# Kernel tuning notes

Hardware: AMD Instinct MI355X
Metric: run time of the kernel (lower is better)

The kernel has to match this reference:

```python
import jax, jax.numpy as jnp
import numpy as np

N_HEAD = 16
D_HEAD = 64
D_MODEL = 1024
N_ROLL = 3
SCALE = 1.0 / (D_HEAD ** 0.5)
EPS = 1e-5


def mul_roll_repeat(x, n_roll):
    # concat of x * roll(x, i) over i=1..n_roll along last dim
    return jnp.concatenate([x * jnp.roll(x, i, axis=-1) for i in range(1, n_roll + 1)], axis=-1)


def dpfp(x):
    # DPFP feature map: [relu(x), relu(-x)] then roll-multiply-repeat
    x2 = jnp.concatenate([jax.nn.relu(x), jax.nn.relu(-x)], axis=-1)
    return mul_roll_repeat(x2, N_ROLL)


def layer_norm(x, gamma, beta):
    mu = jnp.mean(x, axis=-1, keepdims=True)
    var = jnp.var(x, axis=-1, keepdims=True)
    return (x - mu) * jax.lax.rsqrt(var + 1e-5) * gamma + beta


def setup_inputs() -> dict:
    key = jax.random.key(0)
    ks = jax.random.split(key, 4)
    S, B = 2048, 2
    h = jax.random.normal(ks[0], (S, B, D_MODEL), dtype=jnp.float32)
    Wq = jax.random.normal(ks[1], (D_MODEL, N_HEAD * D_HEAD), dtype=jnp.float32) * 0.02
    Wkv = jax.random.normal(ks[2], (D_MODEL, 2 * N_HEAD * D_HEAD), dtype=jnp.float32) * 0.02
    Wo = jax.random.normal(ks[3], (N_HEAD * D_HEAD, D_MODEL), dtype=jnp.float32) * 0.02
    ln_gamma = jnp.ones((D_MODEL,), dtype=jnp.float32)
    ln_beta = jnp.zeros((D_MODEL,), dtype=jnp.float32)
    return {"h": h, "Wq": Wq, "Wkv": Wkv, "Wo": Wo, "ln_gamma": ln_gamma, "ln_beta": ln_beta}


def reference(h, Wq, Wkv, Wo, ln_gamma, ln_beta):
    # h: [S, B, D_MODEL]; mems=None, attn_mask=None, post-LN, eval (no dropout)
    S, B, _ = h.shape
    q = (h @ Wq).reshape(S, B, N_HEAD, D_HEAD)
    kv = h @ Wkv
    k, v = jnp.split(kv, 2, axis=-1)
    k = k.reshape(S, B, N_HEAD, D_HEAD)
    v = v.reshape(S, B, N_HEAD, D_HEAD)

    pq = dpfp(q)  # [S, B, N, F], F = 2*D_HEAD*N_ROLL = 384
    pk = dpfp(k)

    # Linear-attention form: identical math to the original quadratic
    # einsum('ibnd,jbnd->ijbn') * scale, summed over j for the denominator,
    # since there is no mask and dropatt=0. Avoids the O(S^2) score tensor.
    kv_agg = jnp.einsum('jbnf,jbnd->bnfd', pk, v)          # [B, N, F, D]
    z = pk.sum(axis=0)                                      # [B, N, F]
    num = jnp.einsum('ibnf,bnfd->ibnd', pq, kv_agg) * SCALE  # [S, B, N, D]
    den = jnp.einsum('ibnf,bnf->ibn', pq, z) * SCALE + EPS   # [S, B, N]
    attn_vec = (num / den[..., None]).reshape(S, B, N_HEAD * D_HEAD)

    attn_out = attn_vec @ Wo
    return layer_norm(h + attn_out, ln_gamma, ln_beta)
```

## Files before the change

### kernel.cpp

```cpp
#include <hip/hip_runtime.h>
#include <math.h>

#define NH 16
#define DM 1024
#define FEAT 384
#define SB 4096
#define SEQ 2048

static constexpr float SCALE = 0.125f;
static constexpr float EPS = 1e-5f;

typedef __attribute__((ext_vector_type(8))) _Float16 half8;
typedef __attribute__((ext_vector_type(4))) _Float16 half4;
typedef __attribute__((ext_vector_type(4))) float f32x4;

#define AS1 __attribute__((address_space(1)))
#define AS3 __attribute__((address_space(3)))

#define IDX(r, o) ((((r) << 6)) + ((((o) ^ ((r) & 7))) << 3))

__global__ __launch_bounds__(256) void prep_kernel(const float* __restrict__ h,
                                                   const float* __restrict__ Wq,
                                                   const float* __restrict__ Wkv,
                                                   const float* __restrict__ Wo,
                                                   _Float16* __restrict__ h_h,
                                                   _Float16* __restrict__ WqkvT,
                                                   _Float16* __restrict__ WoT) {
    __shared__ _Float16 tile[32][33];
    int bid = blockIdx.x, t = threadIdx.x;
    if (bid < 4096) {
        int i = bid * 256 + t;
        const float4 v = ((const float4*)h)[i];
        half4 o = {(_Float16)v.x, (_Float16)v.y, (_Float16)v.z, (_Float16)v.w};
        ((half4*)h_h)[i] = o;
        return;
    }
    const float* src;
    _Float16* dst;
    int N, col0, n0, k0;
    if (bid < 7168) {
        int b2 = bid - 4096;
        n0 = (b2 % 96) * 32; k0 = (b2 / 96) * 32;
        if (n0 < 1024) { src = Wq; N = 1024; col0 = n0; }
        else           { src = Wkv; N = 2048; col0 = n0 - 1024; }
        dst = WqkvT;
    } else {
        int b3 = bid - 7168;
        n0 = (b3 & 31) * 32; k0 = (b3 >> 5) * 32;
        src = Wo; N = 1024; col0 = n0; dst = WoT;
    }
    int tx = t & 31, ty = t >> 5;
    #pragma unroll
    for (int i = 0; i < 4; ++i)
        tile[ty + i * 8][tx] = (_Float16)src[(size_t)(k0 + ty + i * 8) * N + col0 + tx];
    __syncthreads();
    #pragma unroll
    for (int i = 0; i < 4; ++i)
        dst[(size_t)(n0 + ty + i * 8) * 1024 + k0 + tx] = tile[tx][ty + i * 8];
}

__global__ __launch_bounds__(512) void gemm_qkv(const _Float16* __restrict__ A,
                                                const _Float16* __restrict__ BT,
                                                _Float16* __restrict__ C,
                                                int M, int N, int K) {
    __shared__ _Float16 smem[57344];
    const int t = threadIdx.x;
    const int w = t >> 6, l = t & 63;
    const int wr = w >> 1, wc = w & 1;
    const int NT = K >> 6;

    int nwg = gridDim.x;
    int cpx = nwg >> 3;
    int bid = blockIdx.x;
    int swz = (bid & 7) * cpx + (bid >> 3);
    int ntile = N / 192;
    int row0 = (swz / ntile) << 8;
    int col0 = (swz % ntile) * 192;

    f32x4 acc[4][6];
    #pragma unroll
    for (int m = 0; m < 4; ++m)
        #pragma unroll
        for (int n = 0; n < 6; ++n)
            acc[m][n] = (f32x4){0.f, 0.f, 0.f, 0.f};

    const int lr = l >> 3;
    const int lc8 = ((l & 7) ^ lr) * 8;

    auto STAGE_TILE = [&](int tau) {
        if (tau >= NT) return;
        int kk = tau << 6;
        int bufo = (tau & 1) * 28672;
        #pragma unroll
        for (int i = 0; i < 2; ++i) {
            int chunk = w * 2 + i;
            const _Float16* src = BT + (size_t)(col0 + chunk * 8 + lr) * K + kk + lc8;
            __builtin_amdgcn_global_load_lds((const AS1 void*)src,
                (AS3 void*)(smem + bufo + 16384 + chunk * 512), 16, 0, 0);
        }
        {
            const _Float16* src = BT + (size_t)(col0 + 128 + w * 8 + lr) * K + kk + lc8;
            __builtin_amdgcn_global_load_lds((const AS1 void*)src,
                (AS3 void*)(smem + bufo + 24576 + w * 512), 16, 0, 0);
        }
        #pragma unroll
        for (int i = 0; i < 4; ++i) {
            int chunk = w * 4 + i;
            const _Float16* src = A + (size_t)(row0 + chunk * 8 + lr) * K + kk + lc8;
            __builtin_amdgcn_global_load_lds((const AS1 void*)src,
                (AS3 void*)(smem + bufo + chunk * 512), 16, 0, 0);
        }
    };

    STAGE_TILE(0);
    asm volatile("s_waitcnt vmcnt(0)" ::: "memory");
    __builtin_amdgcn_s_barrier();

    #pragma unroll 1
    for (int ti = 0; ti < NT; ++ti) {
        const int bufo = (ti & 1) * 28672;
        STAGE_TILE(ti + 1);
        half8 a[4][2], bv[6][2];
        #pragma unroll
        for (int mf = 0; mf < 4; ++mf) {
            int r = wr * 64 + mf * 16 + (l & 15);
            #pragma unroll
            for (int ks = 0; ks < 2; ++ks) {
                int c16 = (ks * 4 + (l >> 4)) ^ (r & 7);
                a[mf][ks] = *(const half8*)&smem[bufo + r * 64 + c16 * 8];
            }
        }
        #pragma unroll
        for (int nf = 0; nf < 6; ++nf) {
            int r = wc * 96 + nf * 16 + (l & 15);
            #pragma unroll
            for (int ks = 0; ks < 2; ++ks) {
                int c16 = (ks * 4 + (l >> 4)) ^ (r & 7);
                bv[nf][ks] = *(const half8*)&smem[bufo + 16384 + r * 64 + c16 * 8];
            }
        }
        __builtin_amdgcn_sched_barrier(0);
        asm volatile("s_waitcnt lgkmcnt(0)" ::: "memory");
        __builtin_amdgcn_sched_barrier(0);
        __builtin_amdgcn_s_setprio(1);
        #pragma unroll
        for (int mf = 0; mf < 4; ++mf)
            #pragma unroll
            for (int nf = 0; nf < 6; ++nf)
                #pragma unroll
                for (int ks = 0; ks < 2; ++ks)
                    acc[mf][nf] = __builtin_amdgcn_mfma_f32_16x16x32_f16(
                        a[mf][ks], bv[nf][ks], acc[mf][nf], 0, 0, 0);
        __builtin_amdgcn_s_setprio(0);
        __builtin_amdgcn_sched_barrier(0);
        asm volatile("s_waitcnt vmcnt(0)" ::: "memory");
        __builtin_amdgcn_s_barrier();
    }

    int ocol = l & 15, orow4 = (l >> 4) * 4;
    #pragma unroll
    for (int mf = 0; mf < 4; ++mf)
        #pragma unroll
        for (int nf = 0; nf < 6; ++nf) {
            size_t base = (size_t)(row0 + wr * 64 + mf * 16 + orow4) * N
                        + col0 + wc * 96 + nf * 16 + ocol;
            #pragma unroll
            for (int j = 0; j < 4; ++j)
                C[base + (size_t)j * N] = (_Float16)acc[mf][nf][j];
        }
}

__global__ __launch_bounds__(256) void gemm_wo(const _Float16* __restrict__ A,
                                               const _Float16* __restrict__ BT,
                                               _Float16* __restrict__ C,
                                               int M, int N, int K) {
    __shared__ _Float16 smem[3 * 16384];
    const int t = threadIdx.x;
    const int w = t >> 6, l = t & 63;
    const int wr = w >> 1, wc = w & 1;
    const int NT = K >> 6;
    int row0 = blockIdx.y * 128, col0 = blockIdx.x * 128;

    f32x4 acc[4][4];
    #pragma unroll
    for (int m = 0; m < 4; ++m)
        #pragma unroll
        for (int n = 0; n < 4; ++n)
            acc[m][n] = (f32x4){0.f, 0.f, 0.f, 0.f};

    const int lr = l >> 3;
    const int lc8 = ((l & 7) ^ lr) * 8;

    auto STAGE = [&](int ti) {
        if (ti >= NT) return;
        int kk = ti << 6;
        int bufo = (ti % 3) * 16384;
        #pragma unroll
        for (int i = 0; i < 4; ++i) {
            int chunk = w * 4 + i;
            const _Float16* asrc = A + (size_t)(row0 + chunk * 8 + lr) * K + kk + lc8;
            __builtin_amdgcn_global_load_lds((const AS1 void*)asrc,
                (AS3 void*)(smem + bufo + chunk * 512), 16, 0, 0);
            const _Float16* bsrc = BT + (size_t)(col0 + chunk * 8 + lr) * K + kk + lc8;
            __builtin_amdgcn_global_load_lds((const AS1 void*)bsrc,
                (AS3 void*)(smem + bufo + 8192 + chunk * 512), 16, 0, 0);
        }
    };

    STAGE(0); STAGE(1);
    asm volatile("s_waitcnt vmcnt(8)" ::: "memory");
    __builtin_amdgcn_s_barrier();

    #pragma unroll 1
    for (int ti = 0; ti < NT; ++ti) {
        const int bufo = (ti % 3) * 16384;
        half8 a[4][2], bv[4][2];
        #pragma unroll
        for (int mf = 0; mf < 4; ++mf) {
            int r = wr * 64 + mf * 16 + (l & 15);
            #pragma unroll
            for (int ks = 0; ks < 2; ++ks) {
                int c16 = (ks * 4 + (l >> 4)) ^ (r & 7);
                a[mf][ks] = *(const half8*)&smem[bufo + r * 64 + c16 * 8];
            }
        }
        #pragma unroll
        for (int nf = 0; nf < 4; ++nf) {
            int r = wc * 64 + nf * 16 + (l & 15);
            #pragma unroll
            for (int ks = 0; ks < 2; ++ks) {
                int c16 = (ks * 4 + (l >> 4)) ^ (r & 7);
                bv[nf][ks] = *(const half8*)&smem[bufo + 8192 + r * 64 + c16 * 8];
            }
        }
        STAGE(ti + 2);
        __builtin_amdgcn_sched_barrier(0);
        asm volatile("s_waitcnt lgkmcnt(0)" ::: "memory");
        __builtin_amdgcn_sched_barrier(0);
        __builtin_amdgcn_s_setprio(1);
        #pragma unroll
        for (int mf = 0; mf < 4; ++mf)
            #pragma unroll
            for (int nf = 0; nf < 4; ++nf)
                #pragma unroll
                for (int ks = 0; ks < 2; ++ks)
                    acc[mf][nf] = __builtin_amdgcn_mfma_f32_16x16x32_f16(
                        a[mf][ks], bv[nf][ks], acc[mf][nf], 0, 0, 0);
        __builtin_amdgcn_s_setprio(0);
        __builtin_amdgcn_sched_barrier(0);
        if (ti < NT - 2) asm volatile("s_waitcnt vmcnt(8)" ::: "memory");
        else             asm volatile("s_waitcnt vmcnt(0)" ::: "memory");
        __builtin_amdgcn_s_barrier();
    }

    int ocol = l & 15, orow = (l >> 4) * 4;
    #pragma unroll
    for (int mf = 0; mf < 4; ++mf)
        #pragma unroll
        for (int nf = 0; nf < 4; ++nf) {
            size_t base = (size_t)(row0 + wr * 64 + mf * 16 + orow) * N
                        + col0 + wc * 64 + nf * 16 + ocol;
            #pragma unroll
            for (int j = 0; j < 4; ++j)
                C[base + (size_t)j * N] = (_Float16)acc[mf][nf][j];
        }
}

__global__ __launch_bounds__(512) void kvagg_fused(const _Float16* __restrict__ qkv,
                                                   _Float16* __restrict__ kvp,
                                                   float* __restrict__ zp) {
    __shared__ _Float16 x2s[128 * 64];
    __shared__ _Float16 vTs[64 * 64];
    __shared__ _Float16 pkTs[384 * 64];
    const int t = threadIdx.x;
    const int w = t >> 6, l = t & 63;
    const int bn = blockIdx.x;
    const int jseg = blockIdx.y;
    const int b = bn >> 4, nh = bn & 15;

    f32x4 acc[4][3];
    #pragma unroll
    for (int mf = 0; mf < 4; ++mf)
        #pragma unroll
        for (int nf = 0; nf < 3; ++nf)
            acc[mf][nf] = (f32x4){0.f, 0.f, 0.f, 0.f};
    float zacc[3] = {0.f, 0.f, 0.f};

    const int sc = t & 63;
    const int so = t >> 6;

    #pragma unroll 1
    for (int ch = 0; ch < 4; ++ch) {
        int j0 = jseg * 256 + ch * 64;
        _Float16 kx[8], vx[8];
        #pragma unroll
        for (int e = 0; e < 8; ++e) {
            size_t rb = (size_t)((j0 + so * 8 + e) * 2 + b) * 3072 + nh * 64 + sc;
            kx[e] = qkv[rb + 1024];
            vx[e] = qkv[rb + 2048];
        }
        half8 xlo, xhi, vv;
        #pragma unroll
        for (int e = 0; e < 8; ++e) {
            float kf = (float)kx[e];
            xlo[e] = (_Float16)fmaxf(kf, 0.f);
            xhi[e] = (_Float16)fmaxf(-kf, 0.f);
            vv[e] = vx[e];
        }
        if (ch) __syncthreads();
        *(half8*)&x2s[IDX(sc, so)] = xlo;
        *(half8*)&x2s[IDX(sc + 64, so)] = xhi;
        *(half8*)&vTs[IDX(sc, so)] = vv;
        __syncthreads();
        {
            const int o = t & 7;
            const int fb = t >> 3;
            #pragma unroll
            for (int it = 0; it < 6; ++it) {
                int f = it * 64 + fb;
                int fm = f & 127;
                int r = (f >> 7) + 1;
                int fm2 = (fm - r) & 127;
                half8 pa = *(const half8*)&x2s[IDX(fm, o)];
                half8 pb = *(const half8*)&x2s[IDX(fm2, o)];
                *(half8*)&pkTs[IDX(f, o)] = pa * pb;
            }
        }
        __syncthreads();
        #pragma unroll
        for (int ks = 0; ks < 2; ++ks) {
            half8 a[4], bq[3];
            int oo = ks * 4 + (l >> 4);
            #pragma unroll
            for (int mf = 0; mf < 4; ++mf) {
                int dr = mf * 16 + (l & 15);
                a[mf] = *(const half8*)&vTs[IDX(dr, oo)];
            }
            #pragma unroll
            for (int nf = 0; nf < 3; ++nf) {
                int fr = w * 48 + nf * 16 + (l & 15);
                bq[nf] = *(const half8*)&pkTs[IDX(fr, oo)];
                #pragma unroll
                for (int e = 0; e < 8; ++e) zacc[nf] += (float)bq[nf][e];
            }
            #pragma unroll
            for (int mf = 0; mf < 4; ++mf)
                #pragma unroll
                for (int nf = 0; nf < 3; ++nf)
                    acc[mf][nf] = __builtin_amdgcn_mfma_f32_16x16x32_f16(
                        a[mf], bq[nf], acc[mf][nf], 0, 0, 0);
        }
    }

    #pragma unroll
    for (int nf = 0; nf < 3; ++nf) {
        float v = zacc[nf];
        v += __shfl_xor(v, 16, 64);
        v += __shfl_xor(v, 32, 64);
        if (l < 16)
            zp[(size_t)(jseg * 32 + bn) * FEAT + w * 48 + nf * 16 + l] = v;
    }
    _Float16* outp = kvp + (size_t)(jseg * 32 + bn) * 64 * FEAT;
    int orow = (l >> 4) * 4, ocol = l & 15;
    #pragma unroll
    for (int mf = 0; mf < 4; ++mf)
        #pragma unroll
        for (int nf = 0; nf < 3; ++nf) {
            int fcol = w * 48 + nf * 16 + ocol;
            #pragma unroll
            for (int j = 0; j < 4; ++j)
                outp[(size_t)(mf * 16 + orow + j) * FEAT + fcol] = (_Float16)acc[mf][nf][j];
        }
}

__global__ __launch_bounds__(256) void reduceA(const _Float16* __restrict__ kvp,
                                               const float* __restrict__ zp,
                                               _Float16* __restrict__ kvaggT,
                                               float* __restrict__ z) {
    const int NKV = 32 * 64 * FEAT;
    int idx = blockIdx.x * 256 + threadIdx.x;
    if (idx < NKV) {
        float s = 0.f;
        #pragma unroll
        for (int c = 0; c < 8; ++c) s += (float)kvp[(size_t)c * NKV + idx];
        kvaggT[idx] = (_Float16)s;
    } else if (idx < NKV + 32 * FEAT) {
        int e = idx - NKV;
        float s = 0.f;
        #pragma unroll
        for (int c = 0; c < 8; ++c) s += zp[c * 32 * FEAT + e];
        z[e] = s;
    }
}

#define X2STR 152
__global__ __launch_bounds__(256) void attn_fused(const _Float16* __restrict__ qkv,
                                                  const _Float16* __restrict__ kvaggT,
                                                  const float* __restrict__ z,
                                                  _Float16* __restrict__ av) {
    __shared__ _Float16 x2e[64 * X2STR];
    __shared__ _Float16 B_lds[64 * FEAT];
    __shared__ float z_lds[FEAT];
    __shared__ float den_lds[64];
    const int t = threadIdx.x;
    const int w = t >> 6, l = t & 63;
    const int iblk = blockIdx.x;
    const int bn = blockIdx.y;
    const int b = bn >> 4, nh = bn & 15;

    {
        const _Float16* Bg = kvaggT + (size_t)bn * 64 * FEAT;
        #pragma unroll
        for (int s = 0; s < 12; ++s) {
            int idx8 = t + 256 * s;
            int row = idx8 / 48, c16 = idx8 - row * 48;
            half8 vv = *(const half8*)&Bg[row * FEAT + c16 * 8];
            *(half8*)&B_lds[row * FEAT + ((c16 ^ (row & 7)) << 3)] = vv;
        }
    }
    for (int e = t; e < FEAT; e += 256) z_lds[e] = z[(size_t)bn * FEAT + e];

    {
        int row = t >> 2, c0 = (t & 3) * 16;
        const _Float16* qrow = qkv + (size_t)((iblk * 64 + row) * 2 + b) * 3072 + nh * 64;
        half8 q0 = *(const half8*)&qrow[c0];
        half8 q1 = *(const half8*)&qrow[c0 + 8];
        half8 lo0, lo1, hi0, hi1;
        #pragma unroll
        for (int e = 0; e < 8; ++e) {
            float f0 = (float)q0[e], f1 = (float)q1[e];
            lo0[e] = (_Float16)fmaxf(f0, 0.f);
            lo1[e] = (_Float16)fmaxf(f1, 0.f);
            hi0[e] = (_Float16)fmaxf(-f0, 0.f);
            hi1[e] = (_Float16)fmaxf(-f1, 0.f);
        }
        _Float16* xr = &x2e[row * X2STR];
        *(half8*)&xr[c0] = lo0;
        *(half8*)&xr[c0 + 8] = lo1;
        *(half8*)&xr[64 + c0] = hi0;
        *(half8*)&xr[64 + c0 + 8] = hi1;
        if (c0 == 0) { *(half8*)&xr[128] = lo0; *(half8*)&xr[136] = lo1; }
        if (c0 == 16) { *(half8*)&xr[144] = lo0; }
    }
    __syncthreads();

    const int rloc16 = l & 15;
    const int csel = (l >> 4) * 8;
    const int lrow = w * 16 + rloc16;
    half8 y8[16];
    {
        const _Float16* xr = &x2e[lrow * X2STR + csel];
        #pragma unroll
        for (int j = 0; j < 16; ++j)
            y8[j] = *(const half8*)&xr[j * 8];
    }
    half8 afr[12];
    #pragma unroll
    for (int ks = 0; ks < 12; ++ks) {
        const int r = (ks >> 2) + 1;
        #pragma unroll
        for (int e = 0; e < 8; ++e) {
            const int j1 = ((ks & 3) * 32 + e) & 127;
            const int j2 = ((ks & 3) * 32 + e - r) & 127;
            afr[ks][e] = y8[j1 >> 3][j1 & 7] * y8[j2 >> 3][j2 & 7];
        }
    }

    f32x4 acc[4];
    #pragma unroll
    for (int n = 0; n < 4; ++n) acc[n] = (f32x4){0.f, 0.f, 0.f, 0.f};
    float den = 0.f;
    #pragma unroll
    for (int ks = 0; ks < 12; ++ks) {
        const float4 z0 = *(const float4*)&z_lds[ks * 32 + csel];
        const float4 z1 = *(const float4*)&z_lds[ks * 32 + csel + 4];
        den += (float)afr[ks][0] * z0.x + (float)afr[ks][1] * z0.y
             + (float)afr[ks][2] * z0.z + (float)afr[ks][3] * z0.w
             + (float)afr[ks][4] * z1.x + (float)afr[ks][5] * z1.y
             + (float)afr[ks][6] * z1.z + (float)afr[ks][7] * z1.w;
        #pragma unroll
        for (int nf = 0; nf < 4; ++nf) {
            int row = nf * 16 + rloc16;
            int c16 = (ks * 4 + (l >> 4)) ^ (row & 7);
            half8 bfr = *(const half8*)&B_lds[row * FEAT + (c16 << 3)];
            acc[nf] = __builtin_amdgcn_mfma_f32_16x16x32_f16(afr[ks], bfr, acc[nf], 0, 0, 0);
        }
    }

    den += __shfl_xor(den, 16, 64);
    den += __shfl_xor(den, 32, 64);
    if (l < 16) den_lds[w * 16 + l] = den;
    __syncthreads();

    #pragma unroll
    for (int nf = 0; nf < 4; ++nf)
        #pragma unroll
        for (int j = 0; j < 4; ++j) {
            int rl = w * 16 + (l >> 4) * 4 + j;
            float dv = den_lds[rl] * SCALE + EPS;
            float val = acc[nf][j] * SCALE / dv;
            int i = iblk * 64 + rl;
            av[((size_t)i * 2 + b) * 1024 + nh * 64 + nf * 16 + (l & 15)] = (_Float16)val;
        }
}

__global__ __launch_bounds__(256) void ln_kernel(const float* __restrict__ h,
                                                 const _Float16* __restrict__ attn_out,
                                                 const float* __restrict__ gamma,
                                                 const float* __restrict__ beta,
                                                 float* __restrict__ out) {
    int r = blockIdx.x;
    int t = threadIdx.x;
    const float4 hv = ((const float4*)(h + (size_t)r * 1024))[t];
    const half4 a4 = ((const half4*)(attn_out + (size_t)r * 1024))[t];
    float x[4] = {hv.x + (float)a4[0], hv.y + (float)a4[1],
                  hv.z + (float)a4[2], hv.w + (float)a4[3]};
    float sum = x[0] + x[1] + x[2] + x[3];
    float sq = x[0]*x[0] + x[1]*x[1] + x[2]*x[2] + x[3]*x[3];
    #pragma unroll
    for (int off = 32; off >= 1; off >>= 1) {
        sum += __shfl_xor(sum, off, 64);
        sq += __shfl_xor(sq, off, 64);
    }
    __shared__ float ssum[4], ssq[4];
    int wl = t >> 6, lane = t & 63;
    if (lane == 0) { ssum[wl] = sum; ssq[wl] = sq; }
    __syncthreads();
    sum = ssum[0] + ssum[1] + ssum[2] + ssum[3];
    sq = ssq[0] + ssq[1] + ssq[2] + ssq[3];
    float mu = sum * (1.f / 1024.f);
    float var = sq * (1.f / 1024.f) - mu * mu;
    float rs = rsqrtf(var + 1e-5f);
    const float4 g4 = ((const float4*)gamma)[t];
    const float4 b4 = ((const float4*)beta)[t];
    float4 o;
    o.x = (x[0] - mu) * rs * g4.x + b4.x;
    o.y = (x[1] - mu) * rs * g4.y + b4.y;
    o.z = (x[2] - mu) * rs * g4.z + b4.z;
    o.w = (x[3] - mu) * rs * g4.w + b4.w;
    ((float4*)(out + (size_t)r * 1024))[t] = o;
}

extern "C" void kernel_launch(void* const* d_in, const int* in_sizes, int n_in,
                              void* d_out, int out_size, void* d_ws, size_t ws_size,
                              hipStream_t stream) {
    const float* h     = (const float*)d_in[0];
    const float* Wq    = (const float*)d_in[1];
    const float* Wkv   = (const float*)d_in[2];
    const float* Wo    = (const float*)d_in[3];
    const float* gamma = (const float*)d_in[4];
    const float* beta  = (const float*)d_in[5];
    float* out = (float*)d_out;
    _Float16* u = (_Float16*)d_ws;

    _Float16* h_h    = u;
    _Float16* WqkvT  = u + 4194304;
    _Float16* WoT    = u + 7340032;
    _Float16* qkv    = u + 8388608;
    _Float16* kvp    = u + 20971520;
    float*    zp     = (float*)(u + 33554432);
    _Float16* kvaggT = u + 33751040;
    float*    z      = (float*)(u + 34537472);
    _Float16* av         = h_h;
    _Float16* attn_out_h = qkv;

    dim3 blk(256);
    prep_kernel<<<dim3(8192), blk, 0, stream>>>(h, Wq, Wkv, Wo, h_h, WqkvT, WoT);
    gemm_qkv<<<dim3(256), dim3(512), 0, stream>>>(h_h, WqkvT, qkv, SB, 3072, DM);
    kvagg_fused<<<dim3(32, 8), dim3(512), 0, stream>>>(qkv, kvp, zp);
    reduceA<<<dim3(3120), blk, 0, stream>>>(kvp, zp, kvaggT, z);
    attn_fused<<<dim3(32, 32), blk, 0, stream>>>(qkv, kvaggT, z, av);
    gemm_wo<<<dim3(8, 32), blk, 0, stream>>>(av, WoT, attn_out_h, SB, 1024, DM);
    ln_kernel<<<dim3(SB), blk, 0, stream>>>(h, attn_out_h, gamma, beta, out);
}
```

Measured before the change: 97.95 us.

## Pre-swizzle activations into MFMA fragment layout and load A directly to registers

The prep kernel now converts h to fp16 in a fragment-ordered layout so each lane's MFMA A operand is one contiguous 16-byte load. The QKV GEMM then reads A straight from global memory into double-buffered registers instead of staging it through LDS, which shrinks shared memory to the B tile only. The main loop is unrolled by two, so register buffers aA and aB alternate. This removes the LDS traffic and capacity for A and may allow higher occupancy. The costs are more registers, A loads exposed to global latency, and a loop that assumes an even number of k-tiles.

```diff
diff --git a/kernel.cpp b/kernel.cpp
--- a/kernel.cpp
+++ b/kernel.cpp
@@ -23,29 +23,40 @@
                                                    const float* __restrict__ Wq,
                                                    const float* __restrict__ Wkv,
                                                    const float* __restrict__ Wo,
-                                                   _Float16* __restrict__ h_h,
+                                                   _Float16* __restrict__ hF,
                                                    _Float16* __restrict__ WqkvT,
                                                    _Float16* __restrict__ WoT) {
     __shared__ _Float16 tile[32][33];
     int bid = blockIdx.x, t = threadIdx.x;
-    if (bid < 4096) {
-        int i = bid * 256 + t;
-        const float4 v = ((const float4*)h)[i];
-        half4 o = {(_Float16)v.x, (_Float16)v.y, (_Float16)v.z, (_Float16)v.w};
-        ((half4*)h_h)[i] = o;
+    if (bid < 256) {
+        int rt = bid >> 4, kt = bid & 15;
+        #pragma unroll
+        for (int i = 0; i < 8; ++i) {
+            int tt = t + 256 * i;
+            int g = tt >> 7;
+            int ks = (tt >> 6) & 1;
+            int ll = tt & 63;
+            int row = rt * 256 + g * 16 + (ll & 15);
+            int col = kt * 64 + ks * 32 + (ll >> 4) * 8;
+            const float4 s0 = *(const float4*)&h[(size_t)row * 1024 + col];
+            const float4 s1 = *(const float4*)&h[(size_t)row * 1024 + col + 4];
+            half8 o = {(_Float16)s0.x, (_Float16)s0.y, (_Float16)s0.z, (_Float16)s0.w,
+                       (_Float16)s1.x, (_Float16)s1.y, (_Float16)s1.z, (_Float16)s1.w};
+            *(half8*)&hF[((size_t)(rt * 16 + kt) * 32 + g * 2 + ks) * 512 + ll * 8] = o;
+        }
         return;
     }
     const float* src;
     _Float16* dst;
     int N, col0, n0, k0;
-    if (bid < 7168) {
-        int b2 = bid - 4096;
+    if (bid < 3328) {
+        int b2 = bid - 256;
         n0 = (b2 % 96) * 32; k0 = (b2 / 96) * 32;
         if (n0 < 1024) { src = Wq; N = 1024; col0 = n0; }
         else           { src = Wkv; N = 2048; col0 = n0 - 1024; }
         dst = WqkvT;
     } else {
-        int b3 = bid - 7168;
+        int b3 = bid - 3328;
         n0 = (b3 & 31) * 32; k0 = (b3 >> 5) * 32;
         src = Wo; N = 1024; col0 = n0; dst = WoT;
     }
@@ -59,11 +70,11 @@
         dst[(size_t)(n0 + ty + i * 8) * 1024 + k0 + tx] = tile[tx][ty + i * 8];
 }
 
-__global__ __launch_bounds__(512) void gemm_qkv(const _Float16* __restrict__ A,
+__global__ __launch_bounds__(512) void gemm_qkv(const _Float16* __restrict__ AF,
                                                 const _Float16* __restrict__ BT,
                                                 _Float16* __restrict__ C,
                                                 int M, int N, int K) {
-    __shared__ _Float16 smem[57344];
+    __shared__ _Float16 smem[2 * 12288];
     const int t = threadIdx.x;
     const int w = t >> 6, l = t & 63;
     const int wr = w >> 1, wc = w & 1;
@@ -74,7 +85,8 @@
     int bid = blockIdx.x;
     int swz = (bid & 7) * cpx + (bid >> 3);
     int ntile = N / 192;
-    int row0 = (swz / ntile) << 8;
+    int rt = swz / ntile;
+    int row0 = rt << 8;
     int col0 = (swz % ntile) * 192;
 
     f32x4 acc[4][6];
@@ -87,58 +99,59 @@
     const int lr = l >> 3;
     const int lc8 = ((l & 7) ^ lr) * 8;
 
-    auto STAGE_TILE = [&](int tau) {
+    auto STAGE_B = [&](int tau) {
         if (tau >= NT) return;
         int kk = tau << 6;
-        int bufo = (tau & 1) * 28672;
+        int bufo = (tau & 1) * 12288;
         #pragma unroll
         for (int i = 0; i < 2; ++i) {
             int chunk = w * 2 + i;
             const _Float16* src = BT + (size_t)(col0 + chunk * 8 + lr) * K + kk + lc8;
             __builtin_amdgcn_global_load_lds((const AS1 void*)src,
-                (AS3 void*)(smem + bufo + 16384 + chunk * 512), 16, 0, 0);
+                (AS3 void*)(smem + bufo + chunk * 512), 16, 0, 0);
         }
         {
             const _Float16* src = BT + (size_t)(col0 + 128 + w * 8 + lr) * K + kk + lc8;
             __builtin_amdgcn_global_load_lds((const AS1 void*)src,
-                (AS3 void*)(smem + bufo + 24576 + w * 512), 16, 0, 0);
-        }
-        #pragma unroll
-        for (int i = 0; i < 4; ++i) {
-            int chunk = w * 4 + i;
-            const _Float16* src = A + (size_t)(row0 + chunk * 8 + lr) * K + kk + lc8;
-            __builtin_amdgcn_global_load_lds((const AS1 void*)src,
-                (AS3 void*)(smem + bufo + chunk * 512), 16, 0, 0);
+                (AS3 void*)(smem + bufo + 8192 + w * 512), 16, 0, 0);
         }
     };
 
-    STAGE_TILE(0);
+    const _Float16* afb = AF + (size_t)rt * 16 * 32 * 512;
+    auto LOADA = [&](int tau, half8 (&ar)[4][2]) {
+        if (tau >= NT) return;
+        const _Float16* ap = afb + ((size_t)tau * 32 + wr * 8) * 512 + l * 8;
+        #pragma unroll
+        for (int mf = 0; mf < 4; ++mf)
+            #pragma unroll
+            for (int ks = 0; ks < 2; ++ks)
+                ar[mf][ks] = *(const half8*)&ap[(size_t)(mf * 2 + ks) * 512];
+    };
+
+    auto LDB = [&](int bufo, half8 (&bv)[6][2]) {
+        #pragma unroll
+        for (int nf = 0; nf < 6; ++nf) {
+            int r = wc * 96 + nf * 16 + (l & 15);
+            #pragma unroll
+            for (int ks = 0; ks < 2; ++ks) {
+                int c16 = (ks * 4 + (l >> 4)) ^ (r & 7);
+                bv[nf][ks] = *(const half8*)&smem[bufo + r * 64 + c16 * 8];
+            }
+        }
+    };
+
+    half8 aA[4][2], aB[4][2], bv[6][2];
+
+    LOADA(0, aA);
+    STAGE_B(0);
     asm volatile("s_waitcnt vmcnt(0)" ::: "memory");
     __builtin_amdgcn_s_barrier();
 
     #pragma unroll 1
-    for (int ti = 0; ti < NT; ++ti) {
-        const int bufo = (ti & 1) * 28672;
-        STAGE_TILE(ti + 1);
-        half8 a[4][2], bv[6][2];
-        #pragma unroll
-        for (int mf = 0; mf < 4; ++mf) {
-            int r = wr * 64 + mf * 16 + (l & 15);
-            #pragma unroll
-            for (int ks = 0; ks < 2; ++ks) {
-                int c16 = (ks * 4 + (l >> 4)) ^ (r & 7);
-                a[mf][ks] = *(const half8*)&smem[bufo + r * 64 + c16 * 8];
-            }
-        }
-        #pragma unroll
-        for (int nf = 0; nf < 6; ++nf) {
-            int r = wc * 96 + nf * 16 + (l & 15);
-            #pragma unroll
-            for (int ks = 0; ks < 2; ++ks) {
-                int c16 = (ks * 4 + (l >> 4)) ^ (r & 7);
-                bv[nf][ks] = *(const half8*)&smem[bufo + 16384 + r * 64 + c16 * 8];
-            }
-        }
+    for (int ti = 0; ti < NT; ti += 2) {
+        LOADA(ti + 1, aB);
+        STAGE_B(ti + 1);
+        LDB((ti & 1) * 12288, bv);
         __builtin_amdgcn_sched_barrier(0);
         asm volatile("s_waitcnt lgkmcnt(0)" ::: "memory");
         __builtin_amdgcn_sched_barrier(0);
@@ -150,7 +163,26 @@
                 #pragma unroll
                 for (int ks = 0; ks < 2; ++ks)
                     acc[mf][nf] = __builtin_amdgcn_mfma_f32_16x16x32_f16(
-                        a[mf][ks], bv[nf][ks], acc[mf][nf], 0, 0, 0);
+                        aA[mf][ks], bv[nf][ks], acc[mf][nf], 0, 0, 0);
+        __builtin_amdgcn_s_setprio(0);
+        __builtin_amdgcn_sched_barrier(0);
+        asm volatile("s_waitcnt vmcnt(0)" ::: "memory");
+        __builtin_amdgcn_s_barrier();
+        LOADA(ti + 2, aA);
+        STAGE_B(ti + 2);
+        LDB(((ti + 1) & 1) * 12288, bv);
+        __builtin_amdgcn_sched_barrier(0);
+        asm volatile("s_waitcnt lgkmcnt(0)" ::: "memory");
+        __builtin_amdgcn_sched_barrier(0);
+        __builtin_amdgcn_s_setprio(1);
+        #pragma unroll
+        for (int mf = 0; mf < 4; ++mf)
+            #pragma unroll
+            for (int nf = 0; nf < 6; ++nf)
+                #pragma unroll
+                for (int ks = 0; ks < 2; ++ks)
+                    acc[mf][nf] = __builtin_amdgcn_mfma_f32_16x16x32_f16(
+                        aB[mf][ks], bv[nf][ks], acc[mf][nf], 0, 0, 0);
         __builtin_amdgcn_s_setprio(0);
         __builtin_amdgcn_sched_barrier(0);
         asm volatile("s_waitcnt vmcnt(0)" ::: "memory");
@@ -553,7 +585,7 @@
     float* out = (float*)d_out;
     _Float16* u = (_Float16*)d_ws;
 
-    _Float16* h_h    = u;
+    _Float16* hF     = u;
     _Float16* WqkvT  = u + 4194304;
     _Float16* WoT    = u + 7340032;
     _Float16* qkv    = u + 8388608;
@@ -561,12 +593,12 @@
     float*    zp     = (float*)(u + 33554432);
     _Float16* kvaggT = u + 33751040;
     float*    z      = (float*)(u + 34537472);
-    _Float16* av         = h_h;
+    _Float16* av         = hF;
     _Float16* attn_out_h = qkv;
 
     dim3 blk(256);
-    prep_kernel<<<dim3(8192), blk, 0, stream>>>(h, Wq, Wkv, Wo, h_h, WqkvT, WoT);
-    gemm_qkv<<<dim3(256), dim3(512), 0, stream>>>(h_h, WqkvT, qkv, SB, 3072, DM);
+    prep_kernel<<<dim3(4352), blk, 0, stream>>>(h, Wq, Wkv, Wo, hF, WqkvT, WoT);
+    gemm_qkv<<<dim3(256), dim3(512), 0, stream>>>(hF, WqkvT, qkv, SB, 3072, DM);
     kvagg_fused<<<dim3(32, 8), dim3(512), 0, stream>>>(qkv, kvp, zp);
     reduceA<<<dim3(3120), blk, 0, stream>>>(kvp, zp, kvaggT, z);
     attn_fused<<<dim3(32, 32), blk, 0, stream>>>(qkv, kvaggT, z, av);
```

Measured after the change: 99.56 us. About the same (+1.6%).
